# Kernel optimization log

Hardware: AMD Instinct MI355X
Metric: run time of the kernel (lower is better)

## Reference

```python
import jax, jax.numpy as jnp
import numpy as np

# Dimensions (see shape_source)
R, T, J, F, P, NB = 32, 64, 2048, 4096, 8, 6
H = J + T              # num_heads = 2112
BH = R + T             # num_base_heads = 96
NUM_OUT = H
BATCH = 256
D0, D1 = 96, 96 + F    # diameter columns
S0, S1 = D1, D1 + J    # demand timeseries columns (demand_start = S0)
PS = S1                # static_feat_end == pump_schedules.start
XW = PS + P * 24       # total feature width = 6432


def setup_inputs() -> dict:
    key = jax.random.key(0)
    ks = iter(jax.random.split(key, 64))
    inp = {"x": jax.random.normal(next(ks), (BATCH, XW), jnp.float32),
           "num_steps": 1}

    def lin(name, o, i):
        inp["W_" + name] = jax.random.normal(next(ks), (o, i), jnp.float32) / np.sqrt(i).astype(np.float32)
        inp["b_" + name] = jnp.zeros((o,), jnp.float32)

    def blk(name, o, i):
        inp["W_" + name] = jax.random.normal(next(ks), (NB, o, i), jnp.float32) / np.sqrt(i).astype(np.float32)
        inp["b_" + name] = jnp.zeros((NB, o), jnp.float32)

    lin("h0_q", F, BH)
    lin("h0_h", H, BH)
    lin("S", F, F)
    lin("q0_h", H, F)
    lin("s_q", F, J)
    lin("out", NUM_OUT, F)
    blk("hf", F, H)
    blk("fh", H, F)
    blk("resq", H, F)
    blk("Dq", F, F + P)
    blk("Dh", H, F)
    inp["prelu_a"] = jnp.full((NB,), 0.25, jnp.float32)  # torch PReLU default init
    return inp


def _lin(x, W, b):
    return x @ W.T + b


def reference(x, num_steps, W_h0_q, b_h0_q, W_h0_h, b_h0_h, W_S, b_S,
              W_q0_h, b_q0_h, W_s_q, b_s_q, W_out, b_out,
              W_hf, b_hf, W_fh, b_fh, W_resq, b_resq,
              W_Dq, b_Dq, W_Dh, b_Dh, prelu_a):
    reservoirs = x[:, 0:R]
    tank_levels = x[:, R:R + T]
    d = x[:, D0:D1]
    h0 = jnp.concatenate([reservoirs, tank_levels], axis=1)

    res_h0_q = _lin(h0, W_h0_q, b_h0_q)                 # [B, F]
    res_h0_h = _lin(h0, W_h0_h, b_h0_h)                 # [B, H]
    res_S_q = jax.nn.relu(_lin(d, W_S, b_S))            # [B, F]
    q = (jnp.pi / 4) * d * d                            # [B, F]
    res_q_h = _lin(q, W_q0_h, b_q0_h)                   # [B, H]

    # num_steps == 1: single demand window and pump settings
    s = x[:, S0:S1]                                     # [B, J]
    pump_settings = x[:, PS:PS + P]                     # [B, P]
    res_s_q = _lin(s, W_s_q, b_s_q)                     # [B, F]

    for i in range(NB):
        D_q = _lin(jnp.concatenate([q * res_S_q, pump_settings], axis=1), W_Dq[i], b_Dq[i])
        D_h = jax.nn.relu(_lin(D_q, W_Dh[i], b_Dh[i]))
        hid_x = D_q * (q + res_s_q + res_h0_q)
        h = jax.nn.relu(_lin(hid_x, W_fh[i], b_fh[i]))
        t = _lin((h + res_h0_h + res_q_h) * D_h, W_hf[i], b_hf[i])
        hid_x = jnp.where(t >= 0, t, prelu_a[i] * t)    # PReLU
        q = q - hid_x
        res_q_h = jax.nn.relu(_lin(q, W_resq[i], b_resq[i]))

    return _lin(q, W_out, b_out)                        # [B, NUM_OUT]
```

## Files before the change

### kernel.cpp

```cpp
#include <hip/hip_runtime.h>
#include <stdint.h>

#define XW 6432

typedef unsigned short u16;
typedef __attribute__((ext_vector_type(8))) __bf16 bf16x8;
typedef __attribute__((ext_vector_type(8))) unsigned short us8;
typedef __attribute__((ext_vector_type(4))) float f32x4;

__device__ __forceinline__ u16 f2bf(float x){
  unsigned u = __builtin_bit_cast(unsigned, x);
  u = (u + 0x7FFFu + ((u >> 16) & 1u)) >> 16;
  return (u16)u;
}
__device__ __forceinline__ float bf2f(u16 h){
  unsigned u = ((unsigned)h) << 16;
  return __builtin_bit_cast(float, u);
}
__device__ __forceinline__ void split2(float x, u16 &hi, u16 &lo){
  hi = f2bf(x);
  lo = f2bf(x - bf2f(hi));
}

__launch_bounds__(256, 2)
__global__ void k_gemm(const u16* __restrict__ Ahi, const u16* __restrict__ Alo, int lda,
                       const float* __restrict__ W, int N, int K, int kchunk,
                       float* __restrict__ Cpart)
{
  __shared__ u16 sAh[256*40];
  __shared__ u16 sAl[256*40];
  __shared__ u16 sWh[64*40];
  __shared__ u16 sWl[64*40];

  const int tid  = threadIdx.x;
  const int wid  = tid >> 6;
  const int lane = tid & 63;
  const int n0   = blockIdx.x * 64;
  const int k0   = blockIdx.y * kchunk;
  const int k1   = (k0 + kchunk < K) ? (k0 + kchunk) : K;
  const int nsteps = (k1 - k0 + 31) >> 5;

  f32x4 acc[4][4];
  #pragma unroll
  for (int i=0;i<4;++i)
    #pragma unroll
    for (int j=0;j<4;++j)
      acc[i][j] = f32x4{0.f,0.f,0.f,0.f};

  const int sr = tid >> 2;
  const int sc = (tid & 3) * 8;

  const int colrow = lane & 15;
  const int koff   = (lane >> 4) * 8;

  for (int s=0; s<nsteps; ++s){
    const int kb = k0 + s*32;
    __syncthreads();
    #pragma unroll
    for (int j=0;j<4;++j){
      const int row = j*64 + sr;
      const size_t g = (size_t)row * lda + kb + sc;
      *(us8*)&sAh[row*40 + sc] = *(const us8*)(Ahi + g);
      *(us8*)&sAl[row*40 + sc] = *(const us8*)(Alo + g);
    }
    {
      float v[8];
      const float* wrow = W + (size_t)(n0 + sr) * K;
      if (kb + 32 <= K){
        const float4 p0 = *(const float4*)(wrow + kb + sc);
        const float4 p1 = *(const float4*)(wrow + kb + sc + 4);
        v[0]=p0.x; v[1]=p0.y; v[2]=p0.z; v[3]=p0.w;
        v[4]=p1.x; v[5]=p1.y; v[6]=p1.z; v[7]=p1.w;
      } else {
        #pragma unroll
        for (int jj=0;jj<8;++jj){
          const int k = kb + sc + jj;
          v[jj] = (k < K) ? wrow[k] : 0.f;
        }
      }
      us8 vh, vl;
      #pragma unroll
      for (int jj=0;jj<8;++jj){
        u16 h,l; split2(v[jj],h,l);
        vh[jj]=h; vl[jj]=l;
      }
      *(us8*)&sWh[sr*40 + sc] = vh;
      *(us8*)&sWl[sr*40 + sc] = vl;
    }
    __syncthreads();

    bf16x8 ah[4], al[4], bh[4], bl[4];
    #pragma unroll
    for (int mi=0;mi<4;++mi){
      const int row = wid*64 + mi*16 + colrow;
      ah[mi] = *(const bf16x8*)&sAh[row*40 + koff];
      al[mi] = *(const bf16x8*)&sAl[row*40 + koff];
    }
    #pragma unroll
    for (int ni=0;ni<4;++ni){
      const int row = ni*16 + colrow;
      bh[ni] = *(const bf16x8*)&sWh[row*40 + koff];
      bl[ni] = *(const bf16x8*)&sWl[row*40 + koff];
    }
    #pragma unroll
    for (int mi=0;mi<4;++mi)
      #pragma unroll
      for (int ni=0;ni<4;++ni){
        acc[mi][ni] = __builtin_amdgcn_mfma_f32_16x16x32_bf16(ah[mi], bh[ni], acc[mi][ni], 0,0,0);
        acc[mi][ni] = __builtin_amdgcn_mfma_f32_16x16x32_bf16(ah[mi], bl[ni], acc[mi][ni], 0,0,0);
        acc[mi][ni] = __builtin_amdgcn_mfma_f32_16x16x32_bf16(al[mi], bh[ni], acc[mi][ni], 0,0,0);
      }
  }

  float* outp = Cpart + (size_t)blockIdx.y * 256 * N;
  const int rq = (lane >> 4) * 4;
  #pragma unroll
  for (int mi=0;mi<4;++mi){
    const int rowb = wid*64 + mi*16 + rq;
    #pragma unroll
    for (int ni=0;ni<4;++ni){
      const int col = n0 + ni*16 + colrow;
      #pragma unroll
      for (int r=0;r<4;++r)
        outp[(size_t)(rowb + r) * N + col] = acc[mi][ni][r];
    }
  }
}

__global__ void k_prep0(const float* __restrict__ x,
                        u16* __restrict__ dhi, u16* __restrict__ dlo,
                        float* __restrict__ q, u16* __restrict__ qhi, u16* __restrict__ qlo,
                        u16* __restrict__ shi, u16* __restrict__ slo)
{
  const int idx = blockIdx.x*256 + threadIdx.x;
  const int m = idx >> 12, j = idx & 4095;
  const float d = x[(size_t)m*XW + 96 + j];
  u16 h,l;
  split2(d,h,l); dhi[idx]=h; dlo[idx]=l;
  const float qq = 0.78539816339744830962f * d * d;
  q[idx]=qq; split2(qq,h,l); qhi[idx]=h; qlo[idx]=l;
  if (j < 2048){
    const float sv = x[(size_t)m*XW + 4192 + j];
    split2(sv,h,l);
    const int si = m*2048+j; shi[si]=h; slo[si]=l;
  }
}

__global__ void k_h0(const float* __restrict__ x,
                     const float* __restrict__ Wq, const float* __restrict__ bq,
                     const float* __restrict__ Wh, const float* __restrict__ bh,
                     float* __restrict__ rhq, float* __restrict__ rhh)
{
  __shared__ float xr[16][96];
  const int t = threadIdx.x;
  const int m0 = blockIdx.y * 16;
  for (int i=t; i<16*96; i+=64){
    const int mm=i/96, k=i%96;
    xr[mm][k] = x[(size_t)(m0+mm)*XW + k];
  }
  __syncthreads();
  const int n = blockIdx.x*64 + t;
  float acc[16];
  if (n < 4096){
    const float* w = Wq + (size_t)n*96;
    const float b = bq[n];
    #pragma unroll
    for (int mm=0;mm<16;++mm) acc[mm]=b;
    for (int k=0;k<96;++k){
      const float wv = w[k];
      #pragma unroll
      for (int mm=0;mm<16;++mm) acc[mm] += xr[mm][k]*wv;
    }
    #pragma unroll
    for (int mm=0;mm<16;++mm) rhq[(size_t)(m0+mm)*4096 + n] = acc[mm];
  } else {
    const int nn = n - 4096;
    const float* w = Wh + (size_t)nn*96;
    const float b = bh[nn];
    #pragma unroll
    for (int mm=0;mm<16;++mm) acc[mm]=b;
    for (int k=0;k<96;++k){
      const float wv = w[k];
      #pragma unroll
      for (int mm=0;mm<16;++mm) acc[mm] += xr[mm][k]*wv;
    }
    #pragma unroll
    for (int mm=0;mm<16;++mm) rhh[(size_t)(m0+mm)*2112 + nn] = acc[mm];
  }
}

__global__ void k_cpre(const float* __restrict__ P0, const float* __restrict__ P1,
                       const float* __restrict__ P2,
                       const float* __restrict__ bS, const float* __restrict__ bq0h,
                       const float* __restrict__ bsq,
                       const float* __restrict__ rhq, const float* __restrict__ rhh,
                       const float* __restrict__ q, const float* __restrict__ x,
                       float* __restrict__ resS, float* __restrict__ rsumq,
                       float* __restrict__ rh,
                       u16* __restrict__ A1hi, u16* __restrict__ A1lo)
{
  const int idx = blockIdx.x*256 + threadIdx.x;
  const int m = idx / 4128, j = idx % 4128;
  if (j < 2112){
    float v = bq0h[j];
    #pragma unroll
    for (int s=0;s<8;++s) v += P1[(size_t)s*540672 + m*2112 + j];
    rh[m*2112+j] = rhh[m*2112+j] + v;
  }
  u16 h,l;
  if (j < 4096){
    const int ij = m*4096 + j;
    float vS = bS[j];
    #pragma unroll
    for (int s=0;s<4;++s) vS += P0[(size_t)s*1048576 + ij];
    vS = vS > 0.f ? vS : 0.f;
    resS[ij] = vS;
    float vq = bsq[j];
    #pragma unroll
    for (int s=0;s<4;++s) vq += P2[(size_t)s*1048576 + ij];
    rsumq[ij] = vq + rhq[ij];
    const float a1 = q[ij]*vS;
    split2(a1,h,l); A1hi[m*4128+j]=h; A1lo[m*4128+j]=l;
  } else if (j < 4104){
    const float a1 = x[(size_t)m*XW + 6240 + (j-4096)];
    split2(a1,h,l); A1hi[m*4128+j]=h; A1lo[m*4128+j]=l;
  } else {
    A1hi[m*4128+j]=0; A1lo[m*4128+j]=0;
  }
}

__global__ void k_cd(const float* __restrict__ P0, const float* __restrict__ bDq,
                     const float* __restrict__ q, const float* __restrict__ rsumq,
                     u16* __restrict__ Dqhi, u16* __restrict__ Dqlo,
                     u16* __restrict__ A2hi, u16* __restrict__ A2lo)
{
  const int idx = blockIdx.x*256 + threadIdx.x;
  const int j = idx & 4095;
  float v = bDq[j];
  #pragma unroll
  for (int s=0;s<4;++s) v += P0[(size_t)s*1048576 + idx];
  u16 h,l;
  split2(v,h,l); Dqhi[idx]=h; Dqlo[idx]=l;
  const float a2 = v * (q[idx] + rsumq[idx]);
  split2(a2,h,l); A2hi[idx]=h; A2lo[idx]=l;
}

__global__ void k_ch(const float* __restrict__ P1, const float* __restrict__ P2,
                     const float* __restrict__ bDh, const float* __restrict__ bfh,
                     const float* __restrict__ rh,
                     u16* __restrict__ A3hi, u16* __restrict__ A3lo)
{
  const int idx = blockIdx.x*256 + threadIdx.x;
  const int j = idx % 2112;
  float dh = bDh[j], hh = bfh[j];
  #pragma unroll
  for (int s=0;s<8;++s){
    dh += P1[(size_t)s*540672 + idx];
    hh += P2[(size_t)s*540672 + idx];
  }
  dh = dh > 0.f ? dh : 0.f;
  hh = hh > 0.f ? hh : 0.f;
  const float a3 = (hh + rh[idx]) * dh;
  u16 h,l; split2(a3,h,l); A3hi[idx]=h; A3lo[idx]=l;
}

__global__ void k_cq(const float* __restrict__ P0, const float* __restrict__ bhf,
                     const float* __restrict__ prelu_a, int bi,
                     float* __restrict__ q, const float* __restrict__ resS,
                     u16* __restrict__ qhi, u16* __restrict__ qlo,
                     u16* __restrict__ A1hi, u16* __restrict__ A1lo)
{
  const int idx = blockIdx.x*256 + threadIdx.x;
  const int m = idx >> 12, j = idx & 4095;
  float t = bhf[j];
  #pragma unroll
  for (int s=0;s<4;++s) t += P0[(size_t)s*1048576 + idx];
  const float a = prelu_a[bi];
  const float hid = (t >= 0.f) ? t : a*t;
  const float qn = q[idx] - hid;
  q[idx] = qn;
  u16 h,l;
  split2(qn,h,l); qhi[idx]=h; qlo[idx]=l;
  const float a1 = qn * resS[idx];
  split2(a1,h,l); A1hi[m*4128+j]=h; A1lo[m*4128+j]=l;
}

__global__ void k_cr(const float* __restrict__ P1, const float* __restrict__ bresq,
                     const float* __restrict__ rhh, float* __restrict__ rh)
{
  const int idx = blockIdx.x*256 + threadIdx.x;
  const int j = idx % 2112;
  float v = bresq[j];
  #pragma unroll
  for (int s=0;s<8;++s) v += P1[(size_t)s*540672 + idx];
  v = v > 0.f ? v : 0.f;
  rh[idx] = rhh[idx] + v;
}

__global__ void k_cout(const float* __restrict__ P1, const float* __restrict__ bout,
                       float* __restrict__ outp)
{
  const int idx = blockIdx.x*256 + threadIdx.x;
  const int j = idx % 2112;
  float v = bout[j];
  #pragma unroll
  for (int s=0;s<8;++s) v += P1[(size_t)s*540672 + idx];
  outp[idx] = v;
}

extern "C" void kernel_launch(void* const* d_in, const int* in_sizes, int n_in,
                              void* d_out, int out_size, void* d_ws, size_t ws_size,
                              hipStream_t stream)
{
  const float* x      = (const float*)d_in[0];
  const float* W_h0_q = (const float*)d_in[2];
  const float* b_h0_q = (const float*)d_in[3];
  const float* W_h0_h = (const float*)d_in[4];
  const float* b_h0_h = (const float*)d_in[5];
  const float* W_S    = (const float*)d_in[6];
  const float* b_S    = (const float*)d_in[7];
  const float* W_q0_h = (const float*)d_in[8];
  const float* b_q0_h = (const float*)d_in[9];
  const float* W_s_q  = (const float*)d_in[10];
  const float* b_s_q  = (const float*)d_in[11];
  const float* W_out  = (const float*)d_in[12];
  const float* b_out  = (const float*)d_in[13];
  const float* W_hf   = (const float*)d_in[14];
  const float* b_hf   = (const float*)d_in[15];
  const float* W_fh   = (const float*)d_in[16];
  const float* b_fh   = (const float*)d_in[17];
  const float* W_resq = (const float*)d_in[18];
  const float* b_resq = (const float*)d_in[19];
  const float* W_Dq   = (const float*)d_in[20];
  const float* b_Dq   = (const float*)d_in[21];
  const float* W_Dh   = (const float*)d_in[22];
  const float* b_Dh   = (const float*)d_in[23];
  const float* prelu_a= (const float*)d_in[24];

  char* ws = (char*)d_ws;
  size_t off = 0;
  auto alloc = [&](size_t n)->char*{ char* p = ws + off; off += (n + 255) & ~(size_t)255; return p; };

  u16* A1hi = (u16*)alloc((size_t)256*4128*2);
  u16* A1lo = (u16*)alloc((size_t)256*4128*2);
  u16* qhi  = (u16*)alloc((size_t)256*4096*2);
  u16* qlo  = (u16*)alloc((size_t)256*4096*2);
  u16* dhi  = (u16*)alloc((size_t)256*4096*2);
  u16* dlo  = (u16*)alloc((size_t)256*4096*2);
  u16* shi  = (u16*)alloc((size_t)256*2048*2);
  u16* slo  = (u16*)alloc((size_t)256*2048*2);
  u16* A2hi = (u16*)alloc((size_t)256*4096*2);
  u16* A2lo = (u16*)alloc((size_t)256*4096*2);
  u16* A3hi = (u16*)alloc((size_t)256*2112*2);
  u16* A3lo = (u16*)alloc((size_t)256*2112*2);
  u16* Dqhi = (u16*)alloc((size_t)256*4096*2);
  u16* Dqlo = (u16*)alloc((size_t)256*4096*2);
  float* q     = (float*)alloc((size_t)256*4096*4);
  float* resS  = (float*)alloc((size_t)256*4096*4);
  float* rsumq = (float*)alloc((size_t)256*4096*4);
  float* rh    = (float*)alloc((size_t)256*2112*4);
  float* rhq   = (float*)alloc((size_t)256*4096*4);
  float* rhh   = (float*)alloc((size_t)256*2112*4);
  float* P0    = (float*)alloc((size_t)4*1048576*4);
  float* P1    = (float*)alloc((size_t)8*540672*4);
  float* P2    = (float*)alloc((size_t)8*540672*4);

  k_prep0<<<4096, 256, 0, stream>>>(x, dhi, dlo, q, qhi, qlo, shi, slo);
  k_h0<<<dim3(97,16), 64, 0, stream>>>(x, W_h0_q, b_h0_q, W_h0_h, b_h0_h, rhq, rhh);
  k_gemm<<<dim3(64,4), 256, 0, stream>>>(dhi, dlo, 4096, W_S,    4096, 4096, 1024, P0);
  k_gemm<<<dim3(33,8), 256, 0, stream>>>(qhi, qlo, 4096, W_q0_h, 2112, 4096,  512, P1);
  k_gemm<<<dim3(64,4), 256, 0, stream>>>(shi, slo, 2048, W_s_q,  4096, 2048,  512, P2);
  k_cpre<<<4128, 256, 0, stream>>>(P0, P1, P2, b_S, b_q0_h, b_s_q, rhq, rhh, q, x,
                                   resS, rsumq, rh, A1hi, A1lo);

  for (int i = 0; i < 6; ++i){
    const float* Wdq = W_Dq   + (size_t)i*4096*4104;
    const float* Wdh = W_Dh   + (size_t)i*2112*4096;
    const float* Wfh = W_fh   + (size_t)i*2112*4096;
    const float* Whf = W_hf   + (size_t)i*4096*2112;
    const float* Wrq = W_resq + (size_t)i*2112*4096;

    k_gemm<<<dim3(64,4), 256, 0, stream>>>(A1hi, A1lo, 4128, Wdq, 4096, 4104, 1056, P0);
    k_cd<<<4096, 256, 0, stream>>>(P0, b_Dq + (size_t)i*4096, q, rsumq, Dqhi, Dqlo, A2hi, A2lo);
    k_gemm<<<dim3(33,8), 256, 0, stream>>>(Dqhi, Dqlo, 4096, Wdh, 2112, 4096, 512, P1);
    k_gemm<<<dim3(33,8), 256, 0, stream>>>(A2hi, A2lo, 4096, Wfh, 2112, 4096, 512, P2);
    k_ch<<<2112, 256, 0, stream>>>(P1, P2, b_Dh + (size_t)i*2112, b_fh + (size_t)i*2112, rh, A3hi, A3lo);
    k_gemm<<<dim3(64,4), 256, 0, stream>>>(A3hi, A3lo, 2112, Whf, 4096, 2112, 544, P0);
    k_cq<<<4096, 256, 0, stream>>>(P0, b_hf + (size_t)i*4096, prelu_a, i, q, resS, qhi, qlo, A1hi, A1lo);
    k_gemm<<<dim3(33,8), 256, 0, stream>>>(qhi, qlo, 4096, Wrq, 2112, 4096, 512, P1);
    k_cr<<<2112, 256, 0, stream>>>(P1, b_resq + (size_t)i*2112, rhh, rh);
  }

  k_gemm<<<dim3(33,8), 256, 0, stream>>>(qhi, qlo, 4096, W_out, 2112, 4096, 512, P1);
  k_cout<<<2112, 256, 0, stream>>>(P1, b_out, (float*)d_out);
}
```

Baseline: 2.582 ms.

## Software-pipeline GEMM with register prefetch and double-buffered weight LDS

Restructures the split-bf16 GEMM main loop so the next k-step's A and W tiles are prefetched into registers while the current step computes. A is no longer staged through LDS; each lane loads its MFMA fragments straight from global memory. W is double-buffered in LDS so only one barrier per step is needed. Launch bounds drop the min-2-blocks hint, which allows higher register use at the risk of lower occupancy.

```diff
diff --git a/kernel.cpp b/kernel.cpp
--- a/kernel.cpp
+++ b/kernel.cpp
@@ -22,15 +22,16 @@
   lo = f2bf(x - bf2f(hi));
 }
 
-__launch_bounds__(256, 2)
+struct APref { us8 h[4]; us8 l[4]; };
+struct WPref { float4 w0, w1; };
+
+__launch_bounds__(256)
 __global__ void k_gemm(const u16* __restrict__ Ahi, const u16* __restrict__ Alo, int lda,
                        const float* __restrict__ W, int N, int K, int kchunk,
                        float* __restrict__ Cpart)
 {
-  __shared__ u16 sAh[256*40];
-  __shared__ u16 sAl[256*40];
-  __shared__ u16 sWh[64*40];
-  __shared__ u16 sWl[64*40];
+  __shared__ u16 sWh[2][64*40];
+  __shared__ u16 sWl[2][64*40];
 
   const int tid  = threadIdx.x;
   const int wid  = tid >> 6;
@@ -40,6 +41,12 @@
   const int k1   = (k0 + kchunk < K) ? (k0 + kchunk) : K;
   const int nsteps = (k1 - k0 + 31) >> 5;
 
+  const int sr = tid >> 2;
+  const int sc = (tid & 3) * 8;
+
+  const int colrow = lane & 15;
+  const int koff   = (lane >> 4) * 8;
+
   f32x4 acc[4][4];
   #pragma unroll
   for (int i=0;i<4;++i)
@@ -47,70 +54,77 @@
     for (int j=0;j<4;++j)
       acc[i][j] = f32x4{0.f,0.f,0.f,0.f};
 
-  const int sr = tid >> 2;
-  const int sc = (tid & 3) * 8;
-
-  const int colrow = lane & 15;
-  const int koff   = (lane >> 4) * 8;
-
-  for (int s=0; s<nsteps; ++s){
-    const int kb = k0 + s*32;
-    __syncthreads();
-    #pragma unroll
-    for (int j=0;j<4;++j){
-      const int row = j*64 + sr;
-      const size_t g = (size_t)row * lda + kb + sc;
-      *(us8*)&sAh[row*40 + sc] = *(const us8*)(Ahi + g);
-      *(us8*)&sAl[row*40 + sc] = *(const us8*)(Alo + g);
-    }
+  const u16* Abase_h = Ahi + (size_t)(wid*64 + colrow) * lda + koff;
+  const u16* Abase_l = Alo + (size_t)(wid*64 + colrow) * lda + koff;
+  const float* wrow  = W + (size_t)(n0 + sr) * K;
+
+  auto loadW = [&](WPref& d, int kb){
+    if (kb + 32 <= K){
+      d.w0 = *(const float4*)(wrow + kb + sc);
+      d.w1 = *(const float4*)(wrow + kb + sc + 4);
+    } else {
+      float t[8];
+      #pragma unroll
+      for (int jj=0;jj<8;++jj){
+        const int k = kb + sc + jj;
+        t[jj] = (k < K) ? wrow[k] : 0.f;
+      }
+      d.w0 = float4{t[0],t[1],t[2],t[3]};
+      d.w1 = float4{t[4],t[5],t[6],t[7]};
+    }
+  };
+  auto loadA = [&](APref& d, int kb){
+    #pragma unroll
+    for (int mi=0;mi<4;++mi){
+      d.h[mi] = *(const us8*)(Abase_h + (size_t)(mi*16)*lda + kb);
+      d.l[mi] = *(const us8*)(Abase_l + (size_t)(mi*16)*lda + kb);
+    }
+  };
+
+  auto step = [&](const APref& cA, const WPref& cW, APref& nA, WPref& nW,
+                  int kbn, bool doload, int par){
+    us8 vh, vl;
     {
-      float v[8];
-      const float* wrow = W + (size_t)(n0 + sr) * K;
-      if (kb + 32 <= K){
-        const float4 p0 = *(const float4*)(wrow + kb + sc);
-        const float4 p1 = *(const float4*)(wrow + kb + sc + 4);
-        v[0]=p0.x; v[1]=p0.y; v[2]=p0.z; v[3]=p0.w;
-        v[4]=p1.x; v[5]=p1.y; v[6]=p1.z; v[7]=p1.w;
-      } else {
-        #pragma unroll
-        for (int jj=0;jj<8;++jj){
-          const int k = kb + sc + jj;
-          v[jj] = (k < K) ? wrow[k] : 0.f;
-        }
+      float v[8] = {cW.w0.x, cW.w0.y, cW.w0.z, cW.w0.w,
+                    cW.w1.x, cW.w1.y, cW.w1.z, cW.w1.w};
+      #pragma unroll
+      for (int jj=0;jj<8;++jj){ u16 h,l; split2(v[jj],h,l); vh[jj]=h; vl[jj]=l; }
+    }
+    *(us8*)&sWh[par][sr*40 + sc] = vh;
+    *(us8*)&sWl[par][sr*40 + sc] = vl;
+    if (doload){ loadW(nW, kbn); loadA(nA, kbn); }
+    asm volatile("s_waitcnt lgkmcnt(0)" ::: "memory");
+    __builtin_amdgcn_s_barrier();
+    asm volatile("" ::: "memory");
+    bf16x8 bh[4], bl[4];
+    #pragma unroll
+    for (int ni=0;ni<4;++ni){
+      const int r = ni*16 + colrow;
+      bh[ni] = *(const bf16x8*)&sWh[par][r*40 + koff];
+      bl[ni] = *(const bf16x8*)&sWl[par][r*40 + koff];
+    }
+    #pragma unroll
+    for (int mi=0;mi<4;++mi){
+      const bf16x8 ah = __builtin_bit_cast(bf16x8, cA.h[mi]);
+      const bf16x8 al = __builtin_bit_cast(bf16x8, cA.l[mi]);
+      #pragma unroll
+      for (int ni=0;ni<4;++ni){
+        acc[mi][ni] = __builtin_amdgcn_mfma_f32_16x16x32_bf16(ah, bh[ni], acc[mi][ni], 0,0,0);
+        acc[mi][ni] = __builtin_amdgcn_mfma_f32_16x16x32_bf16(ah, bl[ni], acc[mi][ni], 0,0,0);
+        acc[mi][ni] = __builtin_amdgcn_mfma_f32_16x16x32_bf16(al, bh[ni], acc[mi][ni], 0,0,0);
       }
-      us8 vh, vl;
-      #pragma unroll
-      for (int jj=0;jj<8;++jj){
-        u16 h,l; split2(v[jj],h,l);
-        vh[jj]=h; vl[jj]=l;
-      }
-      *(us8*)&sWh[sr*40 + sc] = vh;
-      *(us8*)&sWl[sr*40 + sc] = vl;
-    }
-    __syncthreads();
-
-    bf16x8 ah[4], al[4], bh[4], bl[4];
-    #pragma unroll
-    for (int mi=0;mi<4;++mi){
-      const int row = wid*64 + mi*16 + colrow;
-      ah[mi] = *(const bf16x8*)&sAh[row*40 + koff];
-      al[mi] = *(const bf16x8*)&sAl[row*40 + koff];
-    }
-    #pragma unroll
-    for (int ni=0;ni<4;++ni){
-      const int row = ni*16 + colrow;
-      bh[ni] = *(const bf16x8*)&sWh[row*40 + koff];
-      bl[ni] = *(const bf16x8*)&sWl[row*40 + koff];
-    }
-    #pragma unroll
-    for (int mi=0;mi<4;++mi)
-      #pragma unroll
-      for (int ni=0;ni<4;++ni){
-        acc[mi][ni] = __builtin_amdgcn_mfma_f32_16x16x32_bf16(ah[mi], bh[ni], acc[mi][ni], 0,0,0);
-        acc[mi][ni] = __builtin_amdgcn_mfma_f32_16x16x32_bf16(ah[mi], bl[ni], acc[mi][ni], 0,0,0);
-        acc[mi][ni] = __builtin_amdgcn_mfma_f32_16x16x32_bf16(al[mi], bh[ni], acc[mi][ni], 0,0,0);
-      }
-  }
+    }
+  };
+
+  APref a0, a1; WPref w0, w1;
+  loadW(w0, k0); loadA(a0, k0);
+  int s = 0;
+  for (; s + 2 <= nsteps; s += 2){
+    step(a0, w0, a1, w1, k0 + (s+1)*32, true, 0);
+    step(a1, w1, a0, w0, k0 + (s+2)*32, (s+2) < nsteps, 1);
+  }
+  if (s < nsteps)
+    step(a0, w0, a1, w1, 0, false, 0);
 
   float* outp = Cpart + (size_t)blockIdx.y * 256 * N;
   const int rq = (lane >> 4) * 4;
```

After: 2.577 ms. No clear change (-0.2%).
